# Kernel optimization log

Measured on AMD Instinct MI355X. Metric: run time of the kernel, lower is better.

The kernel has to match this reference:

```python
import jax, jax.numpy as jnp
import numpy as np

DEPTH, EMBED, HEADS, FF = 4, 512, 8, 2048
POS_SCALE, POS_WEIGHT = 0.1, 1.0
EPS = 1e-5  # torch LayerNorm default


def setup_inputs() -> dict:
    key = jax.random.key(0)
    ks = jax.random.split(key, 6)
    B, L = 8, 1024
    s = 0.02
    x = jax.random.normal(ks[0], (B, L, EMBED), jnp.float32)
    Wqkv = jax.random.normal(ks[1], (DEPTH, 3 * EMBED, EMBED), jnp.float32) * s
    bqkv = jnp.zeros((DEPTH, 3 * EMBED), jnp.float32)
    W1 = jax.random.normal(ks[2], (DEPTH, FF, EMBED), jnp.float32) * s
    b1 = jnp.zeros((DEPTH, FF), jnp.float32)
    W2 = jax.random.normal(ks[3], (DEPTH, EMBED, FF), jnp.float32) * s
    b2 = jnp.zeros((DEPTH, EMBED), jnp.float32)
    g = jnp.ones((DEPTH, EMBED), jnp.float32)
    bt = jnp.zeros((DEPTH, EMBED), jnp.float32)
    return {"input": x, "Wqkv": Wqkv, "bqkv": bqkv, "W1": W1, "b1": b1,
            "W2": W2, "b2": b2, "g1": g, "bt1": bt, "g2": g, "bt2": bt,
            "g3": g, "bt3": bt}


def _ln(x, g, b):
    m = x.mean(-1, keepdims=True)
    v = ((x - m) ** 2).mean(-1, keepdims=True)
    return (x - m) * jax.lax.rsqrt(v + EPS) * g + b


def reference(input, Wqkv, bqkv, W1, b1, W2, b2, g1, bt1, g2, bt2, g3, bt3):
    x = input
    B, L, E = x.shape
    hd = E // HEADS
    pos_idx = jnp.arange(L)
    # additive relative-position bias: exp(-|i-j| * scale) * weight
    pos = jnp.exp(-jnp.abs(pos_idx[:, None] - pos_idx[None, :]).astype(x.dtype) * POS_SCALE) * POS_WEIGHT
    triu = jnp.triu(jnp.ones((L, L), dtype=bool), 1)
    inv_sqrt_hd = jnp.asarray(1.0 / np.sqrt(hd), x.dtype)
    for d in range(DEPTH):
        # --- RelativeMultiheadAttention self-attn block ---
        qkv = jnp.einsum('ble,fe->blf', x, Wqkv[d]) + bqkv[d]
        q = qkv[..., :E].reshape(B, L, HEADS, hd).transpose(0, 2, 1, 3)
        k = qkv[..., E:2 * E].reshape(B, L, HEADS, hd).transpose(0, 2, 1, 3)
        logits = jnp.einsum('bhqd,bhkd->bhqk', q, k) * inv_sqrt_hd
        # nn.MultiheadAttention returns head-AVERAGED softmax weights
        A = jax.nn.softmax(logits, axis=-1).mean(axis=1)  # [B,L,L]
        # torch: attn_logits[triu(attn_logits,1).to(bool)] = -inf (nonzero strict upper)
        A = jnp.where(triu & (A != 0), -jnp.inf, A)
        W = jax.nn.softmax(A + pos[None], axis=-1)
        sa = jnp.einsum('bqk,bke->bqe', W, x)  # value is RAW x (no v-proj/out-proj)
        x = _ln(x + sa, g1[d], bt1[d])
        # --- NoopAttention cross-attn block contributes zeros ---
        x = _ln(x, g2[d], bt2[d])
        # --- FFN block (relu activation, post-norm) ---
        h = jax.nn.relu(jnp.einsum('ble,fe->blf', x, W1[d]) + b1[d])
        ff = jnp.einsum('blf,ef->ble', h, W2[d]) + b2[d]
        x = _ln(x + ff, g3[d], bt3[d])
    return x
```

## Files before the change

kernel.cpp:

```cpp
#include <hip/hip_runtime.h>

#define NB 8
#define SEQ 1024
#define EMB 512
#define FFD 2048
#define NROWS (NB*SEQ)
#define LNEPS 1e-5f

typedef __bf16 bf16x8 __attribute__((ext_vector_type(8)));
typedef float f32x4 __attribute__((ext_vector_type(4)));

__device__ __forceinline__ unsigned short f2bf(float f){
  unsigned u = __builtin_bit_cast(unsigned, f);
  u += 0x7fffu + ((u>>16)&1u);
  return (unsigned short)(u>>16);
}
__device__ __forceinline__ bf16x8 ld_bf8(const unsigned short* p){
  return *(const bf16x8*)p;
}
__device__ __forceinline__ void async_copy16(const void* g, void* l){
  __builtin_amdgcn_global_load_lds((const __attribute__((address_space(1))) unsigned int*)g,
                                   (__attribute__((address_space(3))) unsigned int*)l,
                                   16, 0, 0);
}

__device__ __forceinline__ float2 block_sum2(float a,float b){
  #pragma unroll
  for(int k=32;k>=1;k>>=1){ a += __shfl_xor(a,k,64); b += __shfl_xor(b,k,64); }
  __shared__ float sa[4], sb[4];
  int w = threadIdx.x>>6;
  __syncthreads();
  if((threadIdx.x&63)==0){ sa[w]=a; sb[w]=b; }
  __syncthreads();
  return make_float2(sa[0]+sa[1]+sa[2]+sa[3], sb[0]+sb[1]+sb[2]+sb[3]);
}

template<bool OUTBF16, bool RELU, bool BIAS, bool CAUSAL>
__global__ __launch_bounds__(256) void gemm_bf16(
    const unsigned short* __restrict__ Ag, const unsigned short* __restrict__ Bg,
    const float* __restrict__ bias, void* __restrict__ Cg,
    int K, int lda, int ldb, int ldc,
    long long strA, long long strB, long long strC)
{
  __shared__ unsigned short As[128*32];
  __shared__ unsigned short Bs[128*32];
  const unsigned short* Ab = Ag + blockIdx.z*strA;
  const unsigned short* Bb = Bg + blockIdx.z*strB;
  const int m0 = blockIdx.y*128, n0 = blockIdx.x*128;
  const int t = threadIdx.x;
  const int lane = t & 63, w = t >> 6;
  const int wy = w >> 1, wx = w & 1;
  const int q = lane >> 4, c = lane & 15;
  f32x4 acc[4][4] = {};
  const int kend = CAUSAL ? (m0 + 128) : K;
  const int srow = t >> 2, skoff = (t & 3) * 8;
  for(int k0 = 0; k0 < kend; k0 += 32){
    async_copy16(Ab + (long long)(m0 + srow)*lda + k0 + skoff,      As + srow*32 + skoff);
    async_copy16(Ab + (long long)(m0 + srow + 64)*lda + k0 + skoff, As + (srow+64)*32 + skoff);
    async_copy16(Bb + (long long)(n0 + srow)*ldb + k0 + skoff,      Bs + srow*32 + skoff);
    async_copy16(Bb + (long long)(n0 + srow + 64)*ldb + k0 + skoff, Bs + (srow+64)*32 + skoff);
    __syncthreads();
    bf16x8 af[4], bfr[4];
    #pragma unroll
    for(int fi=0; fi<4; fi++) af[fi]  = ld_bf8(As + (wy*64 + fi*16 + c)*32 + q*8);
    #pragma unroll
    for(int fj=0; fj<4; fj++) bfr[fj] = ld_bf8(Bs + (wx*64 + fj*16 + c)*32 + q*8);
    #pragma unroll
    for(int fi=0; fi<4; fi++)
      #pragma unroll
      for(int fj=0; fj<4; fj++)
        acc[fi][fj] = __builtin_amdgcn_mfma_f32_16x16x32_bf16(af[fi], bfr[fj], acc[fi][fj], 0,0,0);
    __syncthreads();
  }
  #pragma unroll
  for(int fi=0; fi<4; fi++){
    #pragma unroll
    for(int fj=0; fj<4; fj++){
      const int row = m0 + wy*64 + fi*16 + q*4;
      const int col = n0 + wx*64 + fj*16 + c;
      const float bv = (BIAS && blockIdx.z==0) ? bias[col] : 0.f;
      #pragma unroll
      for(int r=0; r<4; r++){
        float v = acc[fi][fj][r] + bv;
        if(RELU) v = fmaxf(v, 0.f);
        long long off = blockIdx.z*strC + (long long)(row+r)*ldc + col;
        if(OUTBF16) ((unsigned short*)Cg)[off] = f2bf(v);
        else        ((float*)Cg)[off] = v;
      }
    }
  }
}

__global__ __launch_bounds__(256) void qk_dsum(
    const unsigned short* __restrict__ qkv, float* __restrict__ dsum)
{
  __shared__ unsigned short As[128*32];
  __shared__ unsigned short Bs[128*32];
  const int bh = blockIdx.z, b = bh >> 3, h = bh & 7;
  const int i0 = blockIdx.y*128, j0 = blockIdx.x*128;
  const unsigned short* Ab = qkv + (long long)b*SEQ*1024 + h*64;
  const unsigned short* Bb = qkv + (long long)b*SEQ*1024 + 512 + h*64;
  const int t = threadIdx.x, lane = t & 63, w = t >> 6;
  const int wy = w >> 1, wx = w & 1, q = lane >> 4, c = lane & 15;
  f32x4 acc[4][4] = {};
  const int srow = t >> 2, skoff = (t & 3) * 8;
  #pragma unroll
  for(int k0 = 0; k0 < 64; k0 += 32){
    async_copy16(Ab + (long long)(i0 + srow)*1024 + k0 + skoff,      As + srow*32 + skoff);
    async_copy16(Ab + (long long)(i0 + srow + 64)*1024 + k0 + skoff, As + (srow+64)*32 + skoff);
    async_copy16(Bb + (long long)(j0 + srow)*1024 + k0 + skoff,      Bs + srow*32 + skoff);
    async_copy16(Bb + (long long)(j0 + srow + 64)*1024 + k0 + skoff, Bs + (srow+64)*32 + skoff);
    __syncthreads();
    bf16x8 af[4], bfr[4];
    #pragma unroll
    for(int fi=0; fi<4; fi++) af[fi]  = ld_bf8(As + (wy*64 + fi*16 + c)*32 + q*8);
    #pragma unroll
    for(int fj=0; fj<4; fj++) bfr[fj] = ld_bf8(Bs + (wx*64 + fj*16 + c)*32 + q*8);
    #pragma unroll
    for(int fi=0; fi<4; fi++)
      #pragma unroll
      for(int fj=0; fj<4; fj++)
        acc[fi][fj] = __builtin_amdgcn_mfma_f32_16x16x32_bf16(af[fi], bfr[fj], acc[fi][fj], 0,0,0);
    __syncthreads();
  }
  #pragma unroll
  for(int fi=0; fi<4; fi++){
    #pragma unroll
    for(int r=0; r<4; r++){
      float s = 0.f;
      #pragma unroll
      for(int fj=0; fj<4; fj++) s += __expf(acc[fi][fj][r]*0.125f);
      s += __shfl_xor(s,1,64); s += __shfl_xor(s,2,64);
      s += __shfl_xor(s,4,64); s += __shfl_xor(s,8,64);
      if(c == 0)
        atomicAdd(&dsum[(long long)bh*SEQ + i0 + wy*64 + fi*16 + q*4 + r], s);
    }
  }
}

__global__ __launch_bounds__(256) void attn_w(
    const unsigned short* __restrict__ qkv, const float* __restrict__ dsum,
    unsigned short* __restrict__ Wm, float* __restrict__ Dsum2)
{
  __shared__ unsigned short As[64*32];
  __shared__ unsigned short Bs[64*32];
  __shared__ float inv8[8][64];
  const int b = blockIdx.y;
  int x = blockIdx.x;
  int it = 0;
  while((it+1)*(it+2)/2 <= x) ++it;
  const int jt = x - it*(it+1)/2;
  const int i0 = it*64, j0 = jt*64;
  const int t = threadIdx.x, lane = t & 63, w = t >> 6;
  const int q = lane >> 4, c = lane & 15;
  for(int u = t; u < 512; u += 256){
    int h = u >> 6, r = u & 63;
    inv8[h][r] = 1.f/(8.f*dsum[((long long)(b*8 + h))*SEQ + i0 + r]);
  }
  const unsigned short* Qb = qkv + (long long)b*SEQ*1024;
  const int srow = t >> 2, skoff = (t & 3) * 8;
  f32x4 at[4] = {};
  for(int h = 0; h < 8; h++){
    f32x4 l[4] = {};
    #pragma unroll
    for(int k0 = 0; k0 < 64; k0 += 32){
      __syncthreads();
      async_copy16(Qb + (long long)(i0 + srow)*1024 + h*64 + k0 + skoff,       As + srow*32 + skoff);
      async_copy16(Qb + (long long)(j0 + srow)*1024 + 512 + h*64 + k0 + skoff, Bs + srow*32 + skoff);
      __syncthreads();
      bf16x8 af = ld_bf8(As + (w*16 + c)*32 + q*8);
      bf16x8 bfr[4];
      #pragma unroll
      for(int fj=0; fj<4; fj++) bfr[fj] = ld_bf8(Bs + (fj*16 + c)*32 + q*8);
      #pragma unroll
      for(int fj=0; fj<4; fj++)
        l[fj] = __builtin_amdgcn_mfma_f32_16x16x32_bf16(af, bfr[fj], l[fj], 0,0,0);
    }
    #pragma unroll
    for(int r=0; r<4; r++){
      float iv = inv8[h][w*16 + q*4 + r];
      #pragma unroll
      for(int fj=0; fj<4; fj++)
        at[fj][r] += __expf(l[fj][r]*0.125f)*iv;
    }
  }
  float Dacc[4] = {};
  #pragma unroll
  for(int fj=0; fj<4; fj++){
    #pragma unroll
    for(int r=0; r<4; r++){
      const int i = i0 + w*16 + q*4 + r;
      const int j = j0 + fj*16 + c;
      float wv = 0.f;
      if(j <= i) wv = __expf(at[fj][r] + __expf((float)(j - i)*0.1f));
      Wm[((long long)(b*SEQ + i))*SEQ + j] = f2bf(wv);
      Dacc[r] += wv;
    }
  }
  #pragma unroll
  for(int r=0; r<4; r++){
    Dacc[r] += __shfl_xor(Dacc[r],1,64); Dacc[r] += __shfl_xor(Dacc[r],2,64);
    Dacc[r] += __shfl_xor(Dacc[r],4,64); Dacc[r] += __shfl_xor(Dacc[r],8,64);
    if(c == 0)
      atomicAdd(&Dsum2[(long long)b*SEQ + i0 + w*16 + q*4 + r], Dacc[r]);
  }
}

__global__ __launch_bounds__(256) void residual_ln2(
    const float* __restrict__ X, const float* __restrict__ SA,
    const float* __restrict__ Dsum2,
    const float* __restrict__ g1, const float* __restrict__ b1,
    const float* __restrict__ g2, const float* __restrict__ b2,
    float* __restrict__ XO, unsigned short* __restrict__ Xb)
{
  const long long row = blockIdx.x;
  const int t = threadIdx.x;
  const float s = 1.f/Dsum2[row];
  float v0 = X[row*EMB + t]       + SA[row*EMB + t]*s;
  float v1 = X[row*EMB + t + 256] + SA[row*EMB + t + 256]*s;
  float2 ss = block_sum2(v0+v1, v0*v0+v1*v1);
  float mean = ss.x*(1.f/EMB);
  float var  = ss.y*(1.f/EMB) - mean*mean;
  float rstd = rsqrtf(var + LNEPS);
  float y0 = (v0-mean)*rstd*g1[t]     + b1[t];
  float y1 = (v1-mean)*rstd*g1[t+256] + b1[t+256];
  ss = block_sum2(y0+y1, y0*y0+y1*y1);
  mean = ss.x*(1.f/EMB);
  var  = ss.y*(1.f/EMB) - mean*mean;
  rstd = rsqrtf(var + LNEPS);
  float o0 = (y0-mean)*rstd*g2[t]     + b2[t];
  float o1 = (y1-mean)*rstd*g2[t+256] + b2[t+256];
  XO[row*EMB + t] = o0;       XO[row*EMB + t + 256] = o1;
  Xb[row*EMB + t] = f2bf(o0); Xb[row*EMB + t + 256] = f2bf(o1);
}

__global__ __launch_bounds__(256) void residual_ln(
    const float* __restrict__ X, const float* __restrict__ R1,
    const float* __restrict__ R2,
    const float* __restrict__ g, const float* __restrict__ b,
    float* __restrict__ XO, unsigned short* __restrict__ Xb,
    unsigned short* __restrict__ XT)
{
  const long long row = blockIdx.x;
  const int t = threadIdx.x;
  float v0 = X[row*EMB + t]       + R1[row*EMB + t]       + R2[row*EMB + t];
  float v1 = X[row*EMB + t + 256] + R1[row*EMB + t + 256] + R2[row*EMB + t + 256];
  float2 ss = block_sum2(v0+v1, v0*v0+v1*v1);
  float mean = ss.x*(1.f/EMB);
  float var  = ss.y*(1.f/EMB) - mean*mean;
  float rstd = rsqrtf(var + LNEPS);
  float o0 = (v0-mean)*rstd*g[t]     + b[t];
  float o1 = (v1-mean)*rstd*g[t+256] + b[t+256];
  XO[row*EMB + t] = o0;       XO[row*EMB + t + 256] = o1;
  Xb[row*EMB + t] = f2bf(o0); Xb[row*EMB + t + 256] = f2bf(o1);
  XT[(long long)t*NROWS + row] = f2bf(o0);
  XT[(long long)(t+256)*NROWS + row] = f2bf(o1);
}

__global__ __launch_bounds__(256) void init_x(
    const float* __restrict__ in, float* __restrict__ XO,
    unsigned short* __restrict__ Xb, unsigned short* __restrict__ XT)
{
  const long long row = blockIdx.x;
  const int t = threadIdx.x;
  float v0 = in[row*EMB + t];
  float v1 = in[row*EMB + t + 256];
  XO[row*EMB + t] = v0;       XO[row*EMB + t + 256] = v1;
  Xb[row*EMB + t] = f2bf(v0); Xb[row*EMB + t + 256] = f2bf(v1);
  XT[(long long)t*NROWS + row] = f2bf(v0);
  XT[(long long)(t+256)*NROWS + row] = f2bf(v1);
}

__global__ __launch_bounds__(256) void cvt_bf16(
    const float* __restrict__ src, unsigned short* __restrict__ dst, long long n)
{
  long long i = ((long long)blockIdx.x*256 + threadIdx.x)*4;
  if(i < n){
    float4 v = *(const float4*)(src + i);
    ushort4 o = make_ushort4(f2bf(v.x), f2bf(v.y), f2bf(v.z), f2bf(v.w));
    *(ushort4*)(dst + i) = o;
  }
}

extern "C" void kernel_launch(void* const* d_in, const int* in_sizes, int n_in,
                              void* d_out, int out_size, void* d_ws, size_t ws_size,
                              hipStream_t stream)
{
  const float* x_in = (const float*)d_in[0];
  const float* Wqkv = (const float*)d_in[1];
  const float* bqkv = (const float*)d_in[2];
  const float* W1   = (const float*)d_in[3];
  const float* b1   = (const float*)d_in[4];
  const float* W2   = (const float*)d_in[5];
  const float* b2   = (const float*)d_in[6];
  const float* g1   = (const float*)d_in[7];
  const float* bt1  = (const float*)d_in[8];
  const float* g2   = (const float*)d_in[9];
  const float* bt2  = (const float*)d_in[10];
  const float* g3   = (const float*)d_in[11];
  const float* bt3  = (const float*)d_in[12];

  float* X = (float*)d_out;

  char* ws = (char*)d_ws;
  unsigned short* qkv    = (unsigned short*)(ws);
  unsigned short* hbuf   = (unsigned short*)(ws + ((size_t)16<<20));
  unsigned short* Wm     = (unsigned short*)(ws + ((size_t)48<<20));
  float*          tmp    = (float*)         (ws + ((size_t)64<<20));
  float*          tmp2   = (float*)         (ws + ((size_t)80<<20));
  unsigned short* Xb     = (unsigned short*)(ws + ((size_t)96<<20));
  unsigned short* XT     = (unsigned short*)(ws + ((size_t)104<<20));
  unsigned short* Wqkvb  = (unsigned short*)(ws + ((size_t)112<<20));
  unsigned short* W1b    = (unsigned short*)(ws + ((size_t)118<<20));
  unsigned short* W2b    = (unsigned short*)(ws + ((size_t)126<<20));
  float*          dsum   = (float*)         (ws + ((size_t)134<<20));
  float*          Dsum2  = (float*)         (ws + ((size_t)134<<20) + (256<<10));

  cvt_bf16<<<3072, 256, 0, stream>>>(Wqkv, Wqkvb, (long long)4*1536*EMB);
  cvt_bf16<<<4096, 256, 0, stream>>>(W1,   W1b,   (long long)4*FFD*EMB);
  cvt_bf16<<<4096, 256, 0, stream>>>(W2,   W2b,   (long long)4*EMB*FFD);
  init_x<<<NROWS, 256, 0, stream>>>(x_in, X, Xb, XT);

  for(int d=0; d<4; d++){
    hipMemsetAsync(dsum, 0, (256<<10) + (32<<10), stream);

    gemm_bf16<true,false,true,false><<<dim3(8, 64, 1), 256, 0, stream>>>(
        Xb, Wqkvb + (size_t)d*1536*EMB, bqkv + (size_t)d*1536, qkv,
        EMB, EMB, EMB, 1024, 0, 0, 0);

    qk_dsum<<<dim3(8, 8, 64), 256, 0, stream>>>(qkv, dsum);

    attn_w<<<dim3(136, NB), 256, 0, stream>>>(qkv, dsum, Wm, Dsum2);

    gemm_bf16<false,false,false,true><<<dim3(4, 8, NB), 256, 0, stream>>>(
        Wm, XT, nullptr, tmp,
        SEQ, SEQ, NROWS, EMB,
        (long long)SEQ*SEQ, 1024, (long long)SEQ*EMB);

    residual_ln2<<<NROWS, 256, 0, stream>>>(X, tmp, Dsum2,
        g1 + d*EMB, bt1 + d*EMB, g2 + d*EMB, bt2 + d*EMB, X, Xb);

    gemm_bf16<true,true,true,false><<<dim3(16, 64, 1), 256, 0, stream>>>(
        Xb, W1b + (size_t)d*FFD*EMB, b1 + (size_t)d*FFD, hbuf,
        EMB, EMB, EMB, FFD, 0, 0, 0);

    gemm_bf16<false,false,true,false><<<dim3(4, 64, 2), 256, 0, stream>>>(
        hbuf, W2b + (size_t)d*EMB*FFD, b2 + (size_t)d*EMB, tmp,
        1024, FFD, FFD, EMB,
        1024, 1024, (long long)NROWS*EMB);

    residual_ln<<<NROWS, 256, 0, stream>>>(X, tmp, tmp2,
        g3 + d*EMB, bt3 + d*EMB, X, Xb, XT);
  }
}
```

Baseline: 1.097 ms.

## Swizzle LDS tiles, use dedicated transpose for XT, narrow causal GEMM tile

```diff
diff --git a/kernel.cpp b/kernel.cpp
--- a/kernel.cpp
+++ b/kernel.cpp
@@ -35,49 +35,54 @@
   return make_float2(sa[0]+sa[1]+sa[2]+sa[3], sb[0]+sb[1]+sb[2]+sb[3]);
 }
 
-template<bool OUTBF16, bool RELU, bool BIAS, bool CAUSAL>
+template<bool OUTBF16, bool RELU, bool BIAS, bool CAUSAL, int NT>
 __global__ __launch_bounds__(256) void gemm_bf16(
     const unsigned short* __restrict__ Ag, const unsigned short* __restrict__ Bg,
     const float* __restrict__ bias, void* __restrict__ Cg,
     int K, int lda, int ldb, int ldc,
     long long strA, long long strB, long long strC)
 {
+  constexpr int NJ = NT/32;
   __shared__ unsigned short As[128*32];
-  __shared__ unsigned short Bs[128*32];
+  __shared__ unsigned short Bs[NT*32];
   const unsigned short* Ab = Ag + blockIdx.z*strA;
   const unsigned short* Bb = Bg + blockIdx.z*strB;
-  const int m0 = blockIdx.y*128, n0 = blockIdx.x*128;
+  const int m0 = blockIdx.y*128, n0 = blockIdx.x*NT;
   const int t = threadIdx.x;
   const int lane = t & 63, w = t >> 6;
   const int wy = w >> 1, wx = w & 1;
   const int q = lane >> 4, c = lane & 15;
-  f32x4 acc[4][4] = {};
+  f32x4 acc[4][NJ] = {};
   const int kend = CAUSAL ? (m0 + 128) : K;
-  const int srow = t >> 2, skoff = (t & 3) * 8;
+  const int srow = t >> 2;
+  const int sk = (t & 3) * 8;
+  const int gk = ((t & 3) ^ ((t >> 3) & 3)) * 8;
+  const int rs = (q ^ ((c >> 1) & 3)) * 8;
   for(int k0 = 0; k0 < kend; k0 += 32){
-    async_copy16(Ab + (long long)(m0 + srow)*lda + k0 + skoff,      As + srow*32 + skoff);
-    async_copy16(Ab + (long long)(m0 + srow + 64)*lda + k0 + skoff, As + (srow+64)*32 + skoff);
-    async_copy16(Bb + (long long)(n0 + srow)*ldb + k0 + skoff,      Bs + srow*32 + skoff);
-    async_copy16(Bb + (long long)(n0 + srow + 64)*ldb + k0 + skoff, Bs + (srow+64)*32 + skoff);
+    async_copy16(Ab + (long long)(m0 + srow)*lda + k0 + gk,      As + srow*32 + sk);
+    async_copy16(Ab + (long long)(m0 + srow + 64)*lda + k0 + gk, As + (srow+64)*32 + sk);
+    async_copy16(Bb + (long long)(n0 + srow)*ldb + k0 + gk,      Bs + srow*32 + sk);
+    if(NT == 128)
+      async_copy16(Bb + (long long)(n0 + srow + 64)*ldb + k0 + gk, Bs + (srow+64)*32 + sk);
     __syncthreads();
-    bf16x8 af[4], bfr[4];
-    #pragma unroll
-    for(int fi=0; fi<4; fi++) af[fi]  = ld_bf8(As + (wy*64 + fi*16 + c)*32 + q*8);
-    #pragma unroll
-    for(int fj=0; fj<4; fj++) bfr[fj] = ld_bf8(Bs + (wx*64 + fj*16 + c)*32 + q*8);
+    bf16x8 af[4], bfr[NJ];
+    #pragma unroll
+    for(int fi=0; fi<4; fi++) af[fi]  = ld_bf8(As + (wy*64 + fi*16 + c)*32 + rs);
+    #pragma unroll
+    for(int fj=0; fj<NJ; fj++) bfr[fj] = ld_bf8(Bs + (wx*(NT/2) + fj*16 + c)*32 + rs);
     #pragma unroll
     for(int fi=0; fi<4; fi++)
       #pragma unroll
-      for(int fj=0; fj<4; fj++)
+      for(int fj=0; fj<NJ; fj++)
         acc[fi][fj] = __builtin_amdgcn_mfma_f32_16x16x32_bf16(af[fi], bfr[fj], acc[fi][fj], 0,0,0);
     __syncthreads();
   }
   #pragma unroll
   for(int fi=0; fi<4; fi++){
     #pragma unroll
-    for(int fj=0; fj<4; fj++){
+    for(int fj=0; fj<NJ; fj++){
       const int row = m0 + wy*64 + fi*16 + q*4;
-      const int col = n0 + wx*64 + fj*16 + c;
+      const int col = n0 + wx*(NT/2) + fj*16 + c;
       const float bv = (BIAS && blockIdx.z==0) ? bias[col] : 0.f;
       #pragma unroll
       for(int r=0; r<4; r++){
@@ -103,19 +108,22 @@
   const int t = threadIdx.x, lane = t & 63, w = t >> 6;
   const int wy = w >> 1, wx = w & 1, q = lane >> 4, c = lane & 15;
   f32x4 acc[4][4] = {};
-  const int srow = t >> 2, skoff = (t & 3) * 8;
+  const int srow = t >> 2;
+  const int sk = (t & 3) * 8;
+  const int gk = ((t & 3) ^ ((t >> 3) & 3)) * 8;
+  const int rs = (q ^ ((c >> 1) & 3)) * 8;
   #pragma unroll
   for(int k0 = 0; k0 < 64; k0 += 32){
-    async_copy16(Ab + (long long)(i0 + srow)*1024 + k0 + skoff,      As + srow*32 + skoff);
-    async_copy16(Ab + (long long)(i0 + srow + 64)*1024 + k0 + skoff, As + (srow+64)*32 + skoff);
-    async_copy16(Bb + (long long)(j0 + srow)*1024 + k0 + skoff,      Bs + srow*32 + skoff);
-    async_copy16(Bb + (long long)(j0 + srow + 64)*1024 + k0 + skoff, Bs + (srow+64)*32 + skoff);
+    async_copy16(Ab + (long long)(i0 + srow)*1024 + k0 + gk,      As + srow*32 + sk);
+    async_copy16(Ab + (long long)(i0 + srow + 64)*1024 + k0 + gk, As + (srow+64)*32 + sk);
+    async_copy16(Bb + (long long)(j0 + srow)*1024 + k0 + gk,      Bs + srow*32 + sk);
+    async_copy16(Bb + (long long)(j0 + srow + 64)*1024 + k0 + gk, Bs + (srow+64)*32 + sk);
     __syncthreads();
     bf16x8 af[4], bfr[4];
     #pragma unroll
-    for(int fi=0; fi<4; fi++) af[fi]  = ld_bf8(As + (wy*64 + fi*16 + c)*32 + q*8);
-    #pragma unroll
-    for(int fj=0; fj<4; fj++) bfr[fj] = ld_bf8(Bs + (wx*64 + fj*16 + c)*32 + q*8);
+    for(int fi=0; fi<4; fi++) af[fi]  = ld_bf8(As + (wy*64 + fi*16 + c)*32 + rs);
+    #pragma unroll
+    for(int fj=0; fj<4; fj++) bfr[fj] = ld_bf8(Bs + (wx*64 + fj*16 + c)*32 + rs);
     #pragma unroll
     for(int fi=0; fi<4; fi++)
       #pragma unroll
@@ -158,20 +166,23 @@
     inv8[h][r] = 1.f/(8.f*dsum[((long long)(b*8 + h))*SEQ + i0 + r]);
   }
   const unsigned short* Qb = qkv + (long long)b*SEQ*1024;
-  const int srow = t >> 2, skoff = (t & 3) * 8;
+  const int srow = t >> 2;
+  const int sk = (t & 3) * 8;
+  const int gk = ((t & 3) ^ ((t >> 3) & 3)) * 8;
+  const int rs = (q ^ ((c >> 1) & 3)) * 8;
   f32x4 at[4] = {};
   for(int h = 0; h < 8; h++){
     f32x4 l[4] = {};
     #pragma unroll
     for(int k0 = 0; k0 < 64; k0 += 32){
       __syncthreads();
-      async_copy16(Qb + (long long)(i0 + srow)*1024 + h*64 + k0 + skoff,       As + srow*32 + skoff);
-      async_copy16(Qb + (long long)(j0 + srow)*1024 + 512 + h*64 + k0 + skoff, Bs + srow*32 + skoff);
+      async_copy16(Qb + (long long)(i0 + srow)*1024 + h*64 + k0 + gk,       As + srow*32 + sk);
+      async_copy16(Qb + (long long)(j0 + srow)*1024 + 512 + h*64 + k0 + gk, Bs + srow*32 + sk);
       __syncthreads();
-      bf16x8 af = ld_bf8(As + (w*16 + c)*32 + q*8);
+      bf16x8 af = ld_bf8(As + (w*16 + c)*32 + rs);
       bf16x8 bfr[4];
       #pragma unroll
-      for(int fj=0; fj<4; fj++) bfr[fj] = ld_bf8(Bs + (fj*16 + c)*32 + q*8);
+      for(int fj=0; fj<4; fj++) bfr[fj] = ld_bf8(Bs + (fj*16 + c)*32 + rs);
       #pragma unroll
       for(int fj=0; fj<4; fj++)
         l[fj] = __builtin_amdgcn_mfma_f32_16x16x32_bf16(af, bfr[fj], l[fj], 0,0,0);
@@ -203,6 +214,34 @@
     Dacc[r] += __shfl_xor(Dacc[r],4,64); Dacc[r] += __shfl_xor(Dacc[r],8,64);
     if(c == 0)
       atomicAdd(&Dsum2[(long long)b*SEQ + i0 + w*16 + q*4 + r], Dacc[r]);
+  }
+}
+
+__global__ __launch_bounds__(256) void transpose_bf16(
+    const unsigned short* __restrict__ src, unsigned short* __restrict__ dst)
+{
+  __shared__ unsigned short tile[64*65];
+  const int bx = blockIdx.x;
+  const int by = blockIdx.y;
+  const int t = threadIdx.x;
+  #pragma unroll
+  for(int p=0; p<2; p++){
+    int idx = t + p*256;
+    int r = idx >> 3, cc = (idx & 7)*8;
+    alignas(16) unsigned short e[8];
+    *(uint4*)e = *(const uint4*)(src + (long long)(by*64 + r)*512 + bx*64 + cc);
+    #pragma unroll
+    for(int u=0; u<8; u++) tile[r*65 + cc + u] = e[u];
+  }
+  __syncthreads();
+  #pragma unroll
+  for(int p=0; p<2; p++){
+    int idx = t + p*256;
+    int r2 = idx >> 3, c2 = (idx & 7)*8;
+    alignas(16) unsigned short e[8];
+    #pragma unroll
+    for(int u=0; u<8; u++) e[u] = tile[(c2+u)*65 + r2];
+    *(uint4*)(dst + (long long)(bx*64 + r2)*8192 + by*64 + c2) = *(const uint4*)e;
   }
 }
 
@@ -238,8 +277,7 @@
     const float* __restrict__ X, const float* __restrict__ R1,
     const float* __restrict__ R2,
     const float* __restrict__ g, const float* __restrict__ b,
-    float* __restrict__ XO, unsigned short* __restrict__ Xb,
-    unsigned short* __restrict__ XT)
+    float* __restrict__ XO, unsigned short* __restrict__ Xb)
 {
   const long long row = blockIdx.x;
   const int t = threadIdx.x;
@@ -253,13 +291,11 @@
   float o1 = (v1-mean)*rstd*g[t+256] + b[t+256];
   XO[row*EMB + t] = o0;       XO[row*EMB + t + 256] = o1;
   Xb[row*EMB + t] = f2bf(o0); Xb[row*EMB + t + 256] = f2bf(o1);
-  XT[(long long)t*NROWS + row] = f2bf(o0);
-  XT[(long long)(t+256)*NROWS + row] = f2bf(o1);
 }
 
 __global__ __launch_bounds__(256) void init_x(
     const float* __restrict__ in, float* __restrict__ XO,
-    unsigned short* __restrict__ Xb, unsigned short* __restrict__ XT)
+    unsigned short* __restrict__ Xb)
 {
   const long long row = blockIdx.x;
   const int t = threadIdx.x;
@@ -267,8 +303,6 @@
   float v1 = in[row*EMB + t + 256];
   XO[row*EMB + t] = v0;       XO[row*EMB + t + 256] = v1;
   Xb[row*EMB + t] = f2bf(v0); Xb[row*EMB + t + 256] = f2bf(v1);
-  XT[(long long)t*NROWS + row] = f2bf(v0);
-  XT[(long long)(t+256)*NROWS + row] = f2bf(v1);
 }
 
 __global__ __launch_bounds__(256) void cvt_bf16(
@@ -280,6 +314,17 @@
     ushort4 o = make_ushort4(f2bf(v.x), f2bf(v.y), f2bf(v.z), f2bf(v.w));
     *(ushort4*)(dst + i) = o;
   }
+}
+
+__global__ __launch_bounds__(256) void cvt_qkv(
+    const float* __restrict__ src, unsigned short* __restrict__ dst)
+{
+  long long i = ((long long)blockIdx.x*256 + threadIdx.x)*4;
+  int layer = (int)(i >> 19);
+  long long within = i & ((1LL<<19)-1);
+  float4 v = *(const float4*)(src + (long long)layer*1536*512 + within);
+  ushort4 o = make_ushort4(f2bf(v.x), f2bf(v.y), f2bf(v.z), f2bf(v.w));
+  *(ushort4*)(dst + i) = o;
 }
 
 extern "C" void kernel_launch(void* const* d_in, const int* in_sizes, int n_in,
@@ -316,23 +361,24 @@
   float*          dsum   = (float*)         (ws + ((size_t)134<<20));
   float*          Dsum2  = (float*)         (ws + ((size_t)134<<20) + (256<<10));
 
-  cvt_bf16<<<3072, 256, 0, stream>>>(Wqkv, Wqkvb, (long long)4*1536*EMB);
-  cvt_bf16<<<4096, 256, 0, stream>>>(W1,   W1b,   (long long)4*FFD*EMB);
-  cvt_bf16<<<4096, 256, 0, stream>>>(W2,   W2b,   (long long)4*EMB*FFD);
-  init_x<<<NROWS, 256, 0, stream>>>(x_in, X, Xb, XT);
+  cvt_qkv<<<2048, 256, 0, stream>>>(Wqkv, Wqkvb);
+  cvt_bf16<<<4096, 256, 0, stream>>>(W1, W1b, (long long)4*FFD*EMB);
+  cvt_bf16<<<4096, 256, 0, stream>>>(W2, W2b, (long long)4*EMB*FFD);
+  init_x<<<NROWS, 256, 0, stream>>>(x_in, X, Xb);
+  transpose_bf16<<<dim3(8,128), 256, 0, stream>>>(Xb, XT);
 
   for(int d=0; d<4; d++){
     hipMemsetAsync(dsum, 0, (256<<10) + (32<<10), stream);
 
-    gemm_bf16<true,false,true,false><<<dim3(8, 64, 1), 256, 0, stream>>>(
-        Xb, Wqkvb + (size_t)d*1536*EMB, bqkv + (size_t)d*1536, qkv,
+    gemm_bf16<true,false,true,false,128><<<dim3(8, 64, 1), 256, 0, stream>>>(
+        Xb, Wqkvb + (size_t)d*1024*EMB, bqkv + (size_t)d*1536, qkv,
         EMB, EMB, EMB, 1024, 0, 0, 0);
 
     qk_dsum<<<dim3(8, 8, 64), 256, 0, stream>>>(qkv, dsum);
 
     attn_w<<<dim3(136, NB), 256, 0, stream>>>(qkv, dsum, Wm, Dsum2);
 
-    gemm_bf16<false,false,false,true><<<dim3(4, 8, NB), 256, 0, stream>>>(
+    gemm_bf16<false,false,false,true,64><<<dim3(8, 8, NB), 256, 0, stream>>>(
         Wm, XT, nullptr, tmp,
         SEQ, SEQ, NROWS, EMB,
         (long long)SEQ*SEQ, 1024, (long long)SEQ*EMB);
@@ -340,16 +386,17 @@
     residual_ln2<<<NROWS, 256, 0, stream>>>(X, tmp, Dsum2,
         g1 + d*EMB, bt1 + d*EMB, g2 + d*EMB, bt2 + d*EMB, X, Xb);
 
-    gemm_bf16<true,true,true,false><<<dim3(16, 64, 1), 256, 0, stream>>>(
+    gemm_bf16<true,true,true,false,128><<<dim3(16, 64, 1), 256, 0, stream>>>(
         Xb, W1b + (size_t)d*FFD*EMB, b1 + (size_t)d*FFD, hbuf,
         EMB, EMB, EMB, FFD, 0, 0, 0);
 
-    gemm_bf16<false,false,true,false><<<dim3(4, 64, 2), 256, 0, stream>>>(
+    gemm_bf16<false,false,true,false,128><<<dim3(4, 64, 2), 256, 0, stream>>>(
         hbuf, W2b + (size_t)d*EMB*FFD, b2 + (size_t)d*EMB, tmp,
         1024, FFD, FFD, EMB,
         1024, 1024, (long long)NROWS*EMB);
 
     residual_ln<<<NROWS, 256, 0, stream>>>(X, tmp, tmp2,
-        g3 + d*EMB, bt3 + d*EMB, X, Xb, XT);
-  }
-}
+        g3 + d*EMB, bt3 + d*EMB, X, Xb);
+    transpose_bf16<<<dim3(8,128), 256, 0, stream>>>(Xb, XT);
+  }
+}
```

After: 997.3 us. 9.1% less time.
